# Kernel tuning notes

Measured on AMD Instinct MI355X. Metric: run time of the kernel, lower is better.

The kernel has to match this reference:

```python
import jax
import jax.numpy as jnp
import numpy as np

# Periodic-boundary copy indices on the padded 18x18 lattice (dst <- src).
# None of the sources is an earlier destination, so one batched gather/scatter is faithful.
DST_R = np.array([1,1,2,3,4,4,6,7,8,10,11,12,14,14,15,16,17,17,16,15,14,14,12,10,8,6,4,4,3,2])
DST_C = np.array([3,5,7,9,10,11,13,13,14,15,15,16,15,16,15,14,13,11,9,7,6,5,3,2,1,0,0,1,1,2])
SRC_R = np.array([13,13,14,15,16,16,6,7,8,10,11,12,2,2,3,4,5,5,4,3,2,2,12,10,8,6,16,16,15,14])
SRC_C = np.array([15,5,7,9,10,11,1,1,2,3,3,4,3,4,3,2,1,11,9,7,6,5,15,14,13,12,12,13,13,14])

# 4x4 kernel sparsity masks (5 taps each)
_UP = np.zeros((4,4), np.float32);    _UP[[0,0,1,2,2],[0,1,1,1,2]] = 1
_LEFT = np.zeros((4,4), np.float32);  _LEFT[[1,2,2,2,3],[1,0,1,2,1]] = 1
_RIGHT = np.zeros((4,4), np.float32); _RIGHT[[1,2,2,2,3],[1,1,2,3,3]] = 1

def _out_mask():
    m = np.ones((16,16), np.float32)
    for i in range(9):
        m[i, 7+i:16] = 0
    for i in range(7):
        m[9+i, 0:i+1] = 0
    m[0,4:7]=0; m[1,6:8]=0; m[2,8]=0; m[3,9]=0
    m[6,12]=0; m[7,13]=0; m[8,14]=0; m[9,14]=0; m[10,14]=0; m[11,15]=0
    m[13:,14:]=0; m[15,13]=0; m[15,7:9]=0; m[13,5]=0; m[14,6]=0
    m[8,0]=0; m[9,1]=0; m[7,0]=0; m[3,0]=0; m[0:3,0:2]=0; m[0,2]=0
    return m
OUT_MASK = _out_mask()

def _conv(x, w, b):
    # kernel 4, stride 2, no padding: [B,C,18,18] -> [B,O,8,8]
    y = jax.lax.conv_general_dilated(x, w, window_strides=(2,2), padding='VALID',
                                     dimension_numbers=('NCHW','OIHW','NCHW'))
    return y + b[None, :, None, None]

def setup_inputs() -> dict:
    key = jax.random.key(0)
    ks = jax.random.split(key, 7)
    B, C, O = 2048, 64, 64
    x = jax.random.normal(ks[0], (B, C, 16, 16), dtype=jnp.float32)
    w_up = jax.random.normal(ks[1], (O, C, 4, 4), dtype=jnp.float32) * 0.05
    b_up = jax.random.normal(ks[2], (O,), dtype=jnp.float32) * 0.05
    w_left = jax.random.normal(ks[3], (O, C, 4, 4), dtype=jnp.float32) * 0.05
    b_left = jax.random.normal(ks[4], (O,), dtype=jnp.float32) * 0.05
    w_right = jax.random.normal(ks[5], (O, C, 4, 4), dtype=jnp.float32) * 0.05
    b_right = jax.random.normal(ks[6], (O,), dtype=jnp.float32) * 0.05
    return {"x": x, "w_up": w_up, "b_up": b_up, "w_left": w_left,
            "b_left": b_left, "w_right": w_right, "b_right": b_right}

def reference(x, w_up, b_up, w_left, b_left, w_right, b_right):
    # 1) zero-pad to 18x18 and apply periodic-boundary indexed copies
    xp = jnp.pad(x, ((0,0),(0,0),(1,1),(1,1)))
    xp = xp.at[:, :, DST_R, DST_C].set(xp[:, :, SRC_R, SRC_C])
    # 2) masked directional convs [B,O,8,8]
    up = _conv(xp, w_up * jnp.asarray(_UP), b_up)
    left = _conv(xp, w_left * jnp.asarray(_LEFT), b_left)
    right = _conv(xp, w_right * jnp.asarray(_RIGHT), b_right)
    # 3) interleave into 16x16: even rows = (up | 0) interleaved cols,
    #    odd rows = (left | right) interleaved cols
    B, O = up.shape[0], up.shape[1]
    out = jnp.zeros((B, O, 16, 16), x.dtype)
    out = out.at[:, :, 0::2, 0::2].set(up)
    out = out.at[:, :, 1::2, 0::2].set(left)
    out = out.at[:, :, 1::2, 1::2].set(right)
    # 4) static zero-out of non-lattice sites
    return out * jnp.asarray(OUT_MASK)
```

## Files before the change

### kernel.cpp

```cpp
#include <hip/hip_runtime.h>
#include <stdint.h>
#include <stddef.h>

typedef __attribute__((ext_vector_type(4))) float    f32x4;
typedef __attribute__((ext_vector_type(4))) uint32_t u32x4;
typedef __attribute__((ext_vector_type(8))) __bf16   bf16x8;

#define CGS   5200
#define NFRAG 15360

__device__ __constant__ uint8_t TAPR[15] = {0,0,1,2,2, 1,2,2,2,3, 1,2,2,2,3};
__device__ __constant__ uint8_t TAPC[15] = {0,1,1,1,2, 1,0,1,2,1, 1,1,2,3,3};

__device__ __constant__ uint8_t PDR[30] = {1,1,2,3,4,4,6,7,8,10,11,12,14,14,15,16,17,17,16,15,14,14,12,10,8,6,4,4,3,2};
__device__ __constant__ uint8_t PDC[30] = {3,5,7,9,10,11,13,13,14,15,15,16,15,16,15,14,13,11,9,7,6,5,3,2,1,0,0,1,1,2};
__device__ __constant__ uint8_t PSR[30] = {13,13,14,15,16,16,6,7,8,10,11,12,2,2,3,4,5,5,4,3,2,2,12,10,8,6,16,16,15,14};
__device__ __constant__ uint8_t PSC[30] = {15,5,7,9,10,11,1,1,2,3,3,4,3,4,3,2,1,11,9,7,6,5,15,14,13,12,12,13,13,14};

__device__ __forceinline__ uint32_t pk2(float a, float b) {
    return (uint32_t)__builtin_bit_cast(uint16_t, (__bf16)a)
         | ((uint32_t)__builtin_bit_cast(uint16_t, (__bf16)b) << 16);
}

__global__ __launch_bounds__(256) void pack_w(const float* __restrict__ wu,
                                              const float* __restrict__ wl,
                                              const float* __restrict__ wr,
                                              uint16_t* __restrict__ pw) {
    int fid = blockIdx.x * 256 + threadIdx.x;
    if (fid >= NFRAG) return;
    int lane = fid & 63;
    int mt   = (fid >> 6) & 3;
    int kk   = (fid >> 8) & 1;
    int td   = fid >> 9;
    const float* w = (td < 5) ? wu : (td < 10) ? wl : wr;
    int o  = mt * 16 + (lane & 15);
    int cb = kk * 32 + (lane >> 4) * 8;
    int kr = TAPR[td], kc = TAPC[td];
    const float* src = w + ((size_t)o * 64 + cb) * 16 + kr * 4 + kc;
    uint32_t d[4];
#pragma unroll
    for (int p = 0; p < 4; ++p)
        d[p] = pk2(src[(2 * p) * 16], src[(2 * p + 1) * 16]);
    u32x4 v = {d[0], d[1], d[2], d[3]};
    *(u32x4*)(pw + (size_t)fid * 8) = v;
}

__device__ __forceinline__ int slotof(int r, int c) { return (c & 1) * 162 + r * 9 + (c >> 1); }

__global__ __launch_bounds__(256, 3) void kagome_main(const float* __restrict__ x,
                                                      const uint16_t* __restrict__ pw,
                                                      const float* __restrict__ bu,
                                                      const float* __restrict__ bl,
                                                      const float* __restrict__ br,
                                                      float* __restrict__ out) {
    __shared__ __align__(16) uint8_t lds[8 * CGS];
    const int tid = threadIdx.x;
    const int b   = blockIdx.x;

    const int l   = tid & 63;
    const int wid = tid >> 6;
    const int q   = l >> 4;
    const int io  = (l >> 3) & 1;
    const int j   = l & 7;

    const int ob = wid * 16 + q * 4;
    f32x4 bias0 = *(const f32x4*)(bu + ob);
    f32x4 bias1 = *(const f32x4*)(bl + ob);
    f32x4 bias2 = *(const f32x4*)(br + ob);

    {
        const float* xb = x + (size_t)b * 16384;
#pragma unroll
        for (int i = 0; i < 2; ++i) {
            const int t    = i * 256 + tid;
            const int cg   = t >> 6;
            const int quad = t & 63;
            const int r0   = quad >> 2;
            const int qc   = quad & 3;
            f32x4 v[8];
#pragma unroll
            for (int ch = 0; ch < 8; ++ch)
                v[ch] = *(const f32x4*)(xb + (cg * 8 + ch) * 256 + quad * 4);
            uint8_t* base = lds + cg * CGS;
#pragma unroll
            for (int e = 0; e < 4; ++e) {
                const int pc   = 4 * qc + e + 1;
                const int slot = slotof(r0 + 1, pc);
                u32x4 w = {pk2(v[0][e], v[1][e]), pk2(v[2][e], v[3][e]),
                           pk2(v[4][e], v[5][e]), pk2(v[6][e], v[7][e])};
                *(u32x4*)(base + slot * 16) = w;
            }
        }
        u32x4 z = {0, 0, 0, 0};
        for (int idx = tid; idx < 68 * 8; idx += 256) {
            int s = idx >> 3, cg = idx & 7;
            int r, c;
            if (s < 18)      { r = 0;  c = s; }
            else if (s < 36) { r = 17; c = s - 18; }
            else             { int k2 = s - 36; r = 1 + (k2 >> 1); c = (k2 & 1) * 17; }
            *(u32x4*)(lds + cg * CGS + slotof(r, c) * 16) = z;
        }
    }
    __syncthreads();
    if (tid < 240) {
        int pair = tid >> 3, cg = tid & 7;
        int sa = slotof(PSR[pair], PSC[pair]);
        int da = slotof(PDR[pair], PDC[pair]);
        u32x4 v = *(const u32x4*)(lds + cg * CGS + sa * 16);
        *(u32x4*)(lds + cg * CGS + da * 16) = v;
    }
    __syncthreads();

    f32x4 acc[3][4];
#pragma unroll
    for (int d2 = 0; d2 < 3; ++d2)
#pragma unroll
        for (int n2 = 0; n2 < 4; ++n2) acc[d2][n2] = (f32x4){0.f, 0.f, 0.f, 0.f};

    const int bbase = q * CGS + io * 288 + j * 16;
    const uint16_t* pwl = pw + (size_t)l * 8;

    constexpr uint32_t RM[16] = {0x0008, 0x003C, 0x00FC, 0x01FE, 0x07FF, 0x0FFF, 0x0FFF, 0x1FFE,
                                 0x3FFE, 0xBFFC, 0xBFFC, 0x7FF8, 0xFFF0, 0x3FC0, 0x3F80, 0x1E00};
    const int odd = j & 1;

#define BRD(dr, dc) __builtin_bit_cast(bf16x8, *(const u32x4*)(lb + ((dc) & 1) * 2592 + (4 * nt + (dr)) * 144 + ((dc) >> 1) * 16))
#define DO_MFMAS(KK)                                                                           \
            bf16x8 b00 = BRD(0, 0);                                                            \
            acc[0][nt] = __builtin_amdgcn_mfma_f32_16x16x32_bf16(aw[0], b00, acc[0][nt], 0, 0, 0); \
            bf16x8 b01 = BRD(0, 1);                                                            \
            acc[0][nt] = __builtin_amdgcn_mfma_f32_16x16x32_bf16(aw[1], b01, acc[0][nt], 0, 0, 0); \
            bf16x8 b11 = BRD(1, 1);                                                            \
            acc[0][nt] = __builtin_amdgcn_mfma_f32_16x16x32_bf16(aw[2],  b11, acc[0][nt], 0, 0, 0); \
            acc[1][nt] = __builtin_amdgcn_mfma_f32_16x16x32_bf16(aw[5],  b11, acc[1][nt], 0, 0, 0); \
            acc[2][nt] = __builtin_amdgcn_mfma_f32_16x16x32_bf16(aw[10], b11, acc[2][nt], 0, 0, 0); \
            bf16x8 b20 = BRD(2, 0);                                                            \
            acc[1][nt] = __builtin_amdgcn_mfma_f32_16x16x32_bf16(aw[6],  b20, acc[1][nt], 0, 0, 0); \
            bf16x8 b21 = BRD(2, 1);                                                            \
            acc[0][nt] = __builtin_amdgcn_mfma_f32_16x16x32_bf16(aw[3],  b21, acc[0][nt], 0, 0, 0); \
            acc[1][nt] = __builtin_amdgcn_mfma_f32_16x16x32_bf16(aw[7],  b21, acc[1][nt], 0, 0, 0); \
            acc[2][nt] = __builtin_amdgcn_mfma_f32_16x16x32_bf16(aw[11], b21, acc[2][nt], 0, 0, 0); \
            bf16x8 b22 = BRD(2, 2);                                                            \
            acc[0][nt] = __builtin_amdgcn_mfma_f32_16x16x32_bf16(aw[4],  b22, acc[0][nt], 0, 0, 0); \
            acc[1][nt] = __builtin_amdgcn_mfma_f32_16x16x32_bf16(aw[8],  b22, acc[1][nt], 0, 0, 0); \
            acc[2][nt] = __builtin_amdgcn_mfma_f32_16x16x32_bf16(aw[12], b22, acc[2][nt], 0, 0, 0); \
            bf16x8 b23 = BRD(2, 3);                                                            \
            acc[2][nt] = __builtin_amdgcn_mfma_f32_16x16x32_bf16(aw[13], b23, acc[2][nt], 0, 0, 0); \
            bf16x8 b31 = BRD(3, 1);                                                            \
            acc[1][nt] = __builtin_amdgcn_mfma_f32_16x16x32_bf16(aw[9],  b31, acc[1][nt], 0, 0, 0); \
            bf16x8 b33 = BRD(3, 3);                                                            \
            acc[2][nt] = __builtin_amdgcn_mfma_f32_16x16x32_bf16(aw[14], b33, acc[2][nt], 0, 0, 0);

    {
        bf16x8 aw[15];
#pragma unroll
        for (int f2 = 0; f2 < 15; ++f2) {
            u32x4 t = *(const u32x4*)(pwl + (size_t)((f2 * 2 + 0) * 4 + wid) * 512);
            aw[f2] = __builtin_bit_cast(bf16x8, t);
        }
        const uint8_t* lb = lds + bbase;
#pragma unroll
        for (int nt = 0; nt < 4; ++nt) {
            DO_MFMAS(0)
        }
    }
    {
        bf16x8 aw[15];
#pragma unroll
        for (int f2 = 0; f2 < 15; ++f2) {
            u32x4 t = *(const u32x4*)(pwl + (size_t)((f2 * 2 + 1) * 4 + wid) * 512);
            aw[f2] = __builtin_bit_cast(bf16x8, t);
        }
        const uint8_t* lb = lds + 4 * CGS + bbase;
#pragma unroll
        for (int nt = 0; nt < 4; ++nt) {
            DO_MFMAS(1)
            const int row_e = 4 * nt + 2 * io;
            const uint32_t me = io ? RM[4 * nt + 2] : RM[4 * nt + 0];
            const uint32_t mo = io ? RM[4 * nt + 3] : RM[4 * nt + 1];
            const uint32_t be  = (me >> (2 * j)) & 1u;
            const uint32_t bo0 = (mo >> (2 * j)) & 1u;
            const uint32_t bo1 = (mo >> (2 * j + 1)) & 1u;
#pragma unroll
            for (int r = 0; r < 4; ++r) {
                int o = ob + r;
                float up = acc[0][nt][r] + bias0[r];
                float lf = acc[1][nt][r] + bias1[r];
                float rt = acc[2][nt][r] + bias2[r];
                up = be  ? up : 0.f;
                lf = bo0 ? lf : 0.f;
                rt = bo1 ? rt : 0.f;
                float up_o = __shfl_xor(up, 1);
                float lf_o = __shfl_xor(lf, 1);
                float rt_o = __shfl_xor(rt, 1);
                f32x4 v;
                v[0] = odd ? lf_o : up;
                v[1] = odd ? rt_o : 0.f;
                v[2] = odd ? lf   : up_o;
                v[3] = odd ? rt   : 0.f;
                float* p = out + (((size_t)b * 64 + o) * 256 + (row_e + odd) * 16 + 4 * (j >> 1));
                __builtin_nontemporal_store(v, (f32x4*)p);
            }
        }
    }
#undef DO_MFMAS
#undef BRD
}

extern "C" void kernel_launch(void* const* d_in, const int* in_sizes, int n_in,
                              void* d_out, int out_size, void* d_ws, size_t ws_size,
                              hipStream_t stream) {
    const float* x  = (const float*)d_in[0];
    const float* wu = (const float*)d_in[1];
    const float* bu = (const float*)d_in[2];
    const float* wl = (const float*)d_in[3];
    const float* bl = (const float*)d_in[4];
    const float* wr = (const float*)d_in[5];
    const float* br = (const float*)d_in[6];
    float* out   = (float*)d_out;
    uint16_t* pw = (uint16_t*)d_ws;

    int B = in_sizes[0] / 16384;
    pack_w<<<(NFRAG + 255) / 256, 256, 0, stream>>>(wu, wl, wr, pw);
    kagome_main<<<B, 256, 0, stream>>>(x, pw, bu, bl, br, out);
}
```

Before: 56.98 us.

## Make main kernel persistent over a fixed grid processing 2-3 batches per block

Replaces the one-block-per-batch launch with a fixed grid of 768 blocks, each looping over two or three consecutive batch samples. Border zeroing and the setup of index and mask constants are hoisted out of the per-sample loop and done once per block. The LDS channel-group stride is also bumped from 5200 to 5248 bytes, likely to change bank mapping. The cost is serialised load, sync and compute inside each block with no overlap between samples, plus possible load imbalance between blocks doing 3 versus 2 samples.

```diff
diff --git a/kernel.cpp b/kernel.cpp
--- a/kernel.cpp
+++ b/kernel.cpp
@@ -6,8 +6,9 @@
 typedef __attribute__((ext_vector_type(4))) uint32_t u32x4;
 typedef __attribute__((ext_vector_type(8))) __bf16   bf16x8;
 
-#define CGS   5200
+#define CGS   5248
 #define NFRAG 15360
+#define GRID  768
 
 __device__ __constant__ uint8_t TAPR[15] = {0,0,1,2,2, 1,2,2,2,3, 1,2,2,2,3};
 __device__ __constant__ uint8_t TAPC[15] = {0,1,1,1,2, 1,0,1,2,1, 1,1,2,3,3};
@@ -52,10 +53,15 @@
                                                       const float* __restrict__ bu,
                                                       const float* __restrict__ bl,
                                                       const float* __restrict__ br,
-                                                      float* __restrict__ out) {
+                                                      float* __restrict__ out,
+                                                      int B) {
     __shared__ __align__(16) uint8_t lds[8 * CGS];
     const int tid = threadIdx.x;
-    const int b   = blockIdx.x;
+    const int bid = blockIdx.x;
+
+    const int x3   = B - 2 * GRID;
+    const int nb   = (bid < x3) ? 3 : 2;
+    const int base = (bid < x3) ? bid * 3 : x3 * 3 + (bid - x3) * 2;
 
     const int l   = tid & 63;
     const int wid = tid >> 6;
@@ -68,29 +74,14 @@
     f32x4 bias1 = *(const f32x4*)(bl + ob);
     f32x4 bias2 = *(const f32x4*)(br + ob);
 
+    const int bbase = q * CGS + io * 288 + j * 16;
+    const uint16_t* pwl = pw + (size_t)l * 8;
+
+    constexpr uint32_t RM[16] = {0x0008, 0x003C, 0x00FC, 0x01FE, 0x07FF, 0x0FFF, 0x0FFF, 0x1FFE,
+                                 0x3FFE, 0xBFFC, 0xBFFC, 0x7FF8, 0xFFF0, 0x3FC0, 0x3F80, 0x1E00};
+    const int odd = j & 1;
+
     {
-        const float* xb = x + (size_t)b * 16384;
-#pragma unroll
-        for (int i = 0; i < 2; ++i) {
-            const int t    = i * 256 + tid;
-            const int cg   = t >> 6;
-            const int quad = t & 63;
-            const int r0   = quad >> 2;
-            const int qc   = quad & 3;
-            f32x4 v[8];
-#pragma unroll
-            for (int ch = 0; ch < 8; ++ch)
-                v[ch] = *(const f32x4*)(xb + (cg * 8 + ch) * 256 + quad * 4);
-            uint8_t* base = lds + cg * CGS;
-#pragma unroll
-            for (int e = 0; e < 4; ++e) {
-                const int pc   = 4 * qc + e + 1;
-                const int slot = slotof(r0 + 1, pc);
-                u32x4 w = {pk2(v[0][e], v[1][e]), pk2(v[2][e], v[3][e]),
-                           pk2(v[4][e], v[5][e]), pk2(v[6][e], v[7][e])};
-                *(u32x4*)(base + slot * 16) = w;
-            }
-        }
         u32x4 z = {0, 0, 0, 0};
         for (int idx = tid; idx < 68 * 8; idx += 256) {
             int s = idx >> 3, cg = idx & 7;
@@ -101,31 +92,49 @@
             *(u32x4*)(lds + cg * CGS + slotof(r, c) * 16) = z;
         }
     }
-    __syncthreads();
-    if (tid < 240) {
-        int pair = tid >> 3, cg = tid & 7;
-        int sa = slotof(PSR[pair], PSC[pair]);
-        int da = slotof(PDR[pair], PDC[pair]);
-        u32x4 v = *(const u32x4*)(lds + cg * CGS + sa * 16);
-        *(u32x4*)(lds + cg * CGS + da * 16) = v;
-    }
-    __syncthreads();
-
-    f32x4 acc[3][4];
-#pragma unroll
-    for (int d2 = 0; d2 < 3; ++d2)
-#pragma unroll
-        for (int n2 = 0; n2 < 4; ++n2) acc[d2][n2] = (f32x4){0.f, 0.f, 0.f, 0.f};
-
-    const int bbase = q * CGS + io * 288 + j * 16;
-    const uint16_t* pwl = pw + (size_t)l * 8;
-
-    constexpr uint32_t RM[16] = {0x0008, 0x003C, 0x00FC, 0x01FE, 0x07FF, 0x0FFF, 0x0FFF, 0x1FFE,
-                                 0x3FFE, 0xBFFC, 0xBFFC, 0x7FF8, 0xFFF0, 0x3FC0, 0x3F80, 0x1E00};
-    const int odd = j & 1;
+
+    for (int it = 0; it < nb; ++it) {
+        const int b = base + it;
+
+        {
+            const float* xb = x + (size_t)b * 16384;
+#pragma unroll
+            for (int i = 0; i < 2; ++i) {
+                const int t    = i * 256 + tid;
+                const int cg   = t >> 6;
+                const int quad = t & 63;
+                const int r0   = quad >> 2;
+                const int qc   = quad & 3;
+                f32x4 v[8];
+#pragma unroll
+                for (int ch = 0; ch < 8; ++ch)
+                    v[ch] = *(const f32x4*)(xb + (cg * 8 + ch) * 256 + quad * 4);
+                uint8_t* base_p = lds + cg * CGS;
+#pragma unroll
+                for (int e = 0; e < 4; ++e) {
+                    const int slot = slotof(r0 + 1, 4 * qc + e + 1);
+                    u32x4 w = {pk2(v[0][e], v[1][e]), pk2(v[2][e], v[3][e]),
+                               pk2(v[4][e], v[5][e]), pk2(v[6][e], v[7][e])};
+                    *(u32x4*)(base_p + slot * 16) = w;
+                }
+            }
+        }
+        __syncthreads();
+        if (tid < 240) {
+            int pair = tid >> 3, cg = tid & 7;
+            u32x4 v = *(const u32x4*)(lds + cg * CGS + slotof(PSR[pair], PSC[pair]) * 16);
+            *(u32x4*)(lds + cg * CGS + slotof(PDR[pair], PDC[pair]) * 16) = v;
+        }
+        __syncthreads();
+
+        f32x4 acc[3][4];
+#pragma unroll
+        for (int d2 = 0; d2 < 3; ++d2)
+#pragma unroll
+            for (int n2 = 0; n2 < 4; ++n2) acc[d2][n2] = (f32x4){0.f, 0.f, 0.f, 0.f};
 
 #define BRD(dr, dc) __builtin_bit_cast(bf16x8, *(const u32x4*)(lb + ((dc) & 1) * 2592 + (4 * nt + (dr)) * 144 + ((dc) >> 1) * 16))
-#define DO_MFMAS(KK)                                                                           \
+#define DO_MFMAS()                                                                             \
             bf16x8 b00 = BRD(0, 0);                                                            \
             acc[0][nt] = __builtin_amdgcn_mfma_f32_16x16x32_bf16(aw[0], b00, acc[0][nt], 0, 0, 0); \
             bf16x8 b01 = BRD(0, 1);                                                            \
@@ -151,60 +160,62 @@
             bf16x8 b33 = BRD(3, 3);                                                            \
             acc[2][nt] = __builtin_amdgcn_mfma_f32_16x16x32_bf16(aw[14], b33, acc[2][nt], 0, 0, 0);
 
-    {
-        bf16x8 aw[15];
-#pragma unroll
-        for (int f2 = 0; f2 < 15; ++f2) {
-            u32x4 t = *(const u32x4*)(pwl + (size_t)((f2 * 2 + 0) * 4 + wid) * 512);
-            aw[f2] = __builtin_bit_cast(bf16x8, t);
-        }
-        const uint8_t* lb = lds + bbase;
-#pragma unroll
-        for (int nt = 0; nt < 4; ++nt) {
-            DO_MFMAS(0)
-        }
-    }
-    {
-        bf16x8 aw[15];
-#pragma unroll
-        for (int f2 = 0; f2 < 15; ++f2) {
-            u32x4 t = *(const u32x4*)(pwl + (size_t)((f2 * 2 + 1) * 4 + wid) * 512);
-            aw[f2] = __builtin_bit_cast(bf16x8, t);
-        }
-        const uint8_t* lb = lds + 4 * CGS + bbase;
-#pragma unroll
-        for (int nt = 0; nt < 4; ++nt) {
-            DO_MFMAS(1)
-            const int row_e = 4 * nt + 2 * io;
-            const uint32_t me = io ? RM[4 * nt + 2] : RM[4 * nt + 0];
-            const uint32_t mo = io ? RM[4 * nt + 3] : RM[4 * nt + 1];
-            const uint32_t be  = (me >> (2 * j)) & 1u;
-            const uint32_t bo0 = (mo >> (2 * j)) & 1u;
-            const uint32_t bo1 = (mo >> (2 * j + 1)) & 1u;
-#pragma unroll
-            for (int r = 0; r < 4; ++r) {
-                int o = ob + r;
-                float up = acc[0][nt][r] + bias0[r];
-                float lf = acc[1][nt][r] + bias1[r];
-                float rt = acc[2][nt][r] + bias2[r];
-                up = be  ? up : 0.f;
-                lf = bo0 ? lf : 0.f;
-                rt = bo1 ? rt : 0.f;
-                float up_o = __shfl_xor(up, 1);
-                float lf_o = __shfl_xor(lf, 1);
-                float rt_o = __shfl_xor(rt, 1);
-                f32x4 v;
-                v[0] = odd ? lf_o : up;
-                v[1] = odd ? rt_o : 0.f;
-                v[2] = odd ? lf   : up_o;
-                v[3] = odd ? rt   : 0.f;
-                float* p = out + (((size_t)b * 64 + o) * 256 + (row_e + odd) * 16 + 4 * (j >> 1));
-                __builtin_nontemporal_store(v, (f32x4*)p);
-            }
-        }
-    }
+        {
+            bf16x8 aw[15];
+#pragma unroll
+            for (int f2 = 0; f2 < 15; ++f2) {
+                u32x4 t = *(const u32x4*)(pwl + (size_t)((f2 * 2 + 0) * 4 + wid) * 512);
+                aw[f2] = __builtin_bit_cast(bf16x8, t);
+            }
+            const uint8_t* lb = lds + bbase;
+#pragma unroll
+            for (int nt = 0; nt < 4; ++nt) {
+                DO_MFMAS()
+            }
+        }
+        {
+            bf16x8 aw[15];
+#pragma unroll
+            for (int f2 = 0; f2 < 15; ++f2) {
+                u32x4 t = *(const u32x4*)(pwl + (size_t)((f2 * 2 + 1) * 4 + wid) * 512);
+                aw[f2] = __builtin_bit_cast(bf16x8, t);
+            }
+            const uint8_t* lb = lds + 4 * CGS + bbase;
+#pragma unroll
+            for (int nt = 0; nt < 4; ++nt) {
+                DO_MFMAS()
+                const int row_e = 4 * nt + 2 * io;
+                const uint32_t me = io ? RM[4 * nt + 2] : RM[4 * nt + 0];
+                const uint32_t mo = io ? RM[4 * nt + 3] : RM[4 * nt + 1];
+                const uint32_t be  = (me >> (2 * j)) & 1u;
+                const uint32_t bo0 = (mo >> (2 * j)) & 1u;
+                const uint32_t bo1 = (mo >> (2 * j + 1)) & 1u;
+#pragma unroll
+                for (int r = 0; r < 4; ++r) {
+                    int o = ob + r;
+                    float up = acc[0][nt][r] + bias0[r];
+                    float lf = acc[1][nt][r] + bias1[r];
+                    float rt = acc[2][nt][r] + bias2[r];
+                    up = be  ? up : 0.f;
+                    lf = bo0 ? lf : 0.f;
+                    rt = bo1 ? rt : 0.f;
+                    float up_o = __shfl_xor(up, 1);
+                    float lf_o = __shfl_xor(lf, 1);
+                    float rt_o = __shfl_xor(rt, 1);
+                    f32x4 v;
+                    v[0] = odd ? lf_o : up;
+                    v[1] = odd ? rt_o : 0.f;
+                    v[2] = odd ? lf   : up_o;
+                    v[3] = odd ? rt   : 0.f;
+                    float* p = out + (((size_t)b * 64 + o) * 256 + (row_e + odd) * 16 + 4 * (j >> 1));
+                    __builtin_nontemporal_store(v, (f32x4*)p);
+                }
+            }
+        }
 #undef DO_MFMAS
 #undef BRD
+        if (it + 1 < nb) __syncthreads();
+    }
 }
 
 extern "C" void kernel_launch(void* const* d_in, const int* in_sizes, int n_in,
@@ -222,5 +233,5 @@
 
     int B = in_sizes[0] / 16384;
     pack_w<<<(NFRAG + 255) / 256, 256, 0, stream>>>(wu, wl, wr, pw);
-    kagome_main<<<B, 256, 0, stream>>>(x, pw, bu, bl, br, out);
-}
+    kagome_main<<<GRID, 256, 0, stream>>>(x, pw, bu, bl, br, out, B);
+}
```

Measured after the change: 89.85 us. 1.58x slower.

## Compact LDS layout by storing only even rows of even columns to raise occupancy

Applied to the files above, without the earlier changes.

The padded-input LDS tile no longer stores even-column entries on odd rows, because the convolution taps never read them. This shrinks the per-channel-group stride from 5200 to 3968 bytes. Launch bounds go from 3 to 5 blocks per SM so more blocks can be resident and hide latency. It adds a branchy slot-address function and a conditional store, and 5 blocks per SM may force register spilling given the 15 bf16x8 weight fragments plus 12 f32x4 accumulators per thread.

```diff
diff --git a/kernel.cpp b/kernel.cpp
--- a/kernel.cpp
+++ b/kernel.cpp
@@ -6,7 +6,8 @@
 typedef __attribute__((ext_vector_type(4))) uint32_t u32x4;
 typedef __attribute__((ext_vector_type(8))) __bf16   bf16x8;
 
-#define CGS   5200
+#define CGS   3968
+#define EVENP 2592
 #define NFRAG 15360
 
 __device__ __constant__ uint8_t TAPR[15] = {0,0,1,2,2, 1,2,2,2,3, 1,2,2,2,3};
@@ -20,6 +21,11 @@
 __device__ __forceinline__ uint32_t pk2(float a, float b) {
     return (uint32_t)__builtin_bit_cast(uint16_t, (__bf16)a)
          | ((uint32_t)__builtin_bit_cast(uint16_t, (__bf16)b) << 16);
+}
+
+__device__ __forceinline__ int slotb(int r, int c) {
+    return (c & 1) ? (r * 144 + (c >> 1) * 16)
+                   : (EVENP + (r >> 1) * 144 + (c >> 1) * 16);
 }
 
 __global__ __launch_bounds__(256) void pack_w(const float* __restrict__ wu,
@@ -45,9 +51,7 @@
     *(u32x4*)(pw + (size_t)fid * 8) = v;
 }
 
-__device__ __forceinline__ int slotof(int r, int c) { return (c & 1) * 162 + r * 9 + (c >> 1); }
-
-__global__ __launch_bounds__(256, 3) void kagome_main(const float* __restrict__ x,
+__global__ __launch_bounds__(256, 5) void kagome_main(const float* __restrict__ x,
                                                       const uint16_t* __restrict__ pw,
                                                       const float* __restrict__ bu,
                                                       const float* __restrict__ bl,
@@ -77,6 +81,7 @@
             const int quad = t & 63;
             const int r0   = quad >> 2;
             const int qc   = quad & 3;
+            const int pr   = r0 + 1;
             f32x4 v[8];
 #pragma unroll
             for (int ch = 0; ch < 8; ++ch)
@@ -84,30 +89,30 @@
             uint8_t* base = lds + cg * CGS;
 #pragma unroll
             for (int e = 0; e < 4; ++e) {
-                const int pc   = 4 * qc + e + 1;
-                const int slot = slotof(r0 + 1, pc);
-                u32x4 w = {pk2(v[0][e], v[1][e]), pk2(v[2][e], v[3][e]),
-                           pk2(v[4][e], v[5][e]), pk2(v[6][e], v[7][e])};
-                *(u32x4*)(base + slot * 16) = w;
+                const int c = 4 * qc + e + 1;
+                if ((c & 1) || !(pr & 1)) {
+                    u32x4 w = {pk2(v[0][e], v[1][e]), pk2(v[2][e], v[3][e]),
+                               pk2(v[4][e], v[5][e]), pk2(v[6][e], v[7][e])};
+                    *(u32x4*)(base + slotb(pr, c)) = w;
+                }
             }
         }
         u32x4 z = {0, 0, 0, 0};
-        for (int idx = tid; idx < 68 * 8; idx += 256) {
+        for (int idx = tid; idx < 51 * 8; idx += 256) {
             int s = idx >> 3, cg = idx & 7;
             int r, c;
             if (s < 18)      { r = 0;  c = s; }
-            else if (s < 36) { r = 17; c = s - 18; }
-            else             { int k2 = s - 36; r = 1 + (k2 >> 1); c = (k2 & 1) * 17; }
-            *(u32x4*)(lds + cg * CGS + slotof(r, c) * 16) = z;
+            else if (s < 27) { r = 17; c = 2 * (s - 18) + 1; }
+            else if (s < 35) { r = 2 * (s - 27) + 2; c = 0; }
+            else             { r = s - 35 + 1; c = 17; }
+            *(u32x4*)(lds + cg * CGS + slotb(r, c)) = z;
         }
     }
     __syncthreads();
     if (tid < 240) {
         int pair = tid >> 3, cg = tid & 7;
-        int sa = slotof(PSR[pair], PSC[pair]);
-        int da = slotof(PDR[pair], PDC[pair]);
-        u32x4 v = *(const u32x4*)(lds + cg * CGS + sa * 16);
-        *(u32x4*)(lds + cg * CGS + da * 16) = v;
+        u32x4 v = *(const u32x4*)(lds + cg * CGS + slotb(PSR[pair], PSC[pair]));
+        *(u32x4*)(lds + cg * CGS + slotb(PDR[pair], PDC[pair])) = v;
     }
     __syncthreads();
 
@@ -117,15 +122,16 @@
 #pragma unroll
         for (int n2 = 0; n2 < 4; ++n2) acc[d2][n2] = (f32x4){0.f, 0.f, 0.f, 0.f};
 
-    const int bbase = q * CGS + io * 288 + j * 16;
     const uint16_t* pwl = pw + (size_t)l * 8;
 
     constexpr uint32_t RM[16] = {0x0008, 0x003C, 0x00FC, 0x01FE, 0x07FF, 0x0FFF, 0x0FFF, 0x1FFE,
                                  0x3FFE, 0xBFFC, 0xBFFC, 0x7FF8, 0xFFF0, 0x3FC0, 0x3F80, 0x1E00};
     const int odd = j & 1;
 
-#define BRD(dr, dc) __builtin_bit_cast(bf16x8, *(const u32x4*)(lb + ((dc) & 1) * 2592 + (4 * nt + (dr)) * 144 + ((dc) >> 1) * 16))
-#define DO_MFMAS(KK)                                                                           \
+#define BRD(dr, dc) __builtin_bit_cast(bf16x8, ((dc) & 1)                                      \
+        ? *(const u32x4*)(lb_o + (4 * nt + (dr)) * 144 + ((dc) >> 1) * 16)                     \
+        : *(const u32x4*)(lb_e + (2 * nt + ((dr) >> 1)) * 144 + ((dc) >> 1) * 16))
+#define DO_MFMAS()                                                                             \
             bf16x8 b00 = BRD(0, 0);                                                            \
             acc[0][nt] = __builtin_amdgcn_mfma_f32_16x16x32_bf16(aw[0], b00, acc[0][nt], 0, 0, 0); \
             bf16x8 b01 = BRD(0, 1);                                                            \
@@ -158,10 +164,11 @@
             u32x4 t = *(const u32x4*)(pwl + (size_t)((f2 * 2 + 0) * 4 + wid) * 512);
             aw[f2] = __builtin_bit_cast(bf16x8, t);
         }
-        const uint8_t* lb = lds + bbase;
+        const uint8_t* lb_o = lds + q * CGS + io * 288 + j * 16;
+        const uint8_t* lb_e = lds + q * CGS + EVENP + io * 144 + j * 16;
 #pragma unroll
         for (int nt = 0; nt < 4; ++nt) {
-            DO_MFMAS(0)
+            DO_MFMAS()
         }
     }
     {
@@ -171,10 +178,11 @@
             u32x4 t = *(const u32x4*)(pwl + (size_t)((f2 * 2 + 1) * 4 + wid) * 512);
             aw[f2] = __builtin_bit_cast(bf16x8, t);
         }
-        const uint8_t* lb = lds + 4 * CGS + bbase;
+        const uint8_t* lb_o = lds + (4 + q) * CGS + io * 288 + j * 16;
+        const uint8_t* lb_e = lds + (4 + q) * CGS + EVENP + io * 144 + j * 16;
 #pragma unroll
         for (int nt = 0; nt < 4; ++nt) {
-            DO_MFMAS(1)
+            DO_MFMAS()
             const int row_e = 4 * nt + 2 * io;
             const uint32_t me = io ? RM[4 * nt + 2] : RM[4 * nt + 0];
             const uint32_t mo = io ? RM[4 * nt + 3] : RM[4 * nt + 1];
```

Result: slower. 82.09 us (+44.1%).
